# Kernel optimization log

Measured on AMD Instinct MI355X. Metric: run time of the kernel, lower is better.

The kernel has to match this reference:

```python
import jax, jax.numpy as jnp
import numpy as np

N_QUBITS = 8
N_LAYERS = 3
STATE_DIM = 2 ** N_QUBITS
BATCH = 16384


def _ry(angle):
    # angle: scalar or (B,) -> (2,2) or (B,2,2) complex64 RY matrix
    c = jnp.cos(angle / 2)
    s = jnp.sin(angle / 2)
    return jnp.stack([jnp.stack([c, -s], -1), jnp.stack([s, c], -1)], -2).astype(jnp.complex64)


def _rz(angle):
    # scalar angle -> (2,2) complex64 diag(e^{-i a/2}, e^{i a/2})
    return jnp.diag(jnp.stack([jnp.exp(-1j * angle / 2), jnp.exp(1j * angle / 2)])).astype(jnp.complex64)


def _apply_gate(state, qubit, gate):
    # state: (B, STATE_DIM) complex64; gate: (2,2) or (B,2,2) complex64
    # qubit 0 is the most-significant bit (matches torch view [B,2,...,2])
    B = state.shape[0]
    left = 2 ** qubit
    right = STATE_DIM // (2 * left)
    s = state.reshape(B, left, 2, right)
    if gate.ndim == 3:
        s = jnp.einsum('bst,batr->basr', gate, s)
    else:
        s = jnp.einsum('st,batr->basr', gate, s)
    return s.reshape(B, STATE_DIM)


def _cnot(state, control, target):
    # swap amplitudes with target bit flipped where control bit == 1;
    # identity when target == control (torch skips that case).
    idx = jnp.arange(STATE_DIM)
    cbit = (idx >> (N_QUBITS - 1 - control)) & 1
    tmask = jnp.left_shift(1, N_QUBITS - 1 - target)
    perm = jnp.where(cbit == 1, jnp.bitwise_xor(idx, tmask), idx)
    perm = jnp.where(target == control, idx, perm)
    return state[:, perm]


def _circuit(x, theta, omega, attn_w):
    B = x.shape[0]
    state = jnp.zeros((B, STATE_DIM), jnp.complex64).at[:, 0].set(1.0)
    # amplitude-angle encoding: per-sample RY on each qubit
    for i in range(N_QUBITS):
        state = _apply_gate(state, i, _ry(x[:, i]))
    # CNOT targets from softmax-argmax of entangle attention rows
    targets = jnp.argmax(jax.nn.softmax(attn_w, axis=1), axis=1)  # (N_QUBITS,)
    for layer in range(N_LAYERS):
        for i in range(N_QUBITS):
            state = _apply_gate(state, i, _ry(theta[layer, i]))
        for i in range(N_QUBITS):
            state = _cnot(state, i, targets[i])
        for i in range(N_QUBITS):
            state = _apply_gate(state, i, _rz(omega[layer, i]))
    return state


def setup_inputs() -> dict:
    key = jax.random.key(0)
    k1, k2, k3, k4 = jax.random.split(key, 4)
    x = jax.random.uniform(k1, (BATCH, N_QUBITS), jnp.float32) * np.float32(np.pi)
    theta = jax.random.normal(k2, (N_LAYERS, N_QUBITS), jnp.float32) * 0.1
    omega = jax.random.normal(k3, (N_LAYERS, N_QUBITS), jnp.float32) * 0.1
    # orthogonal init like nn.init.orthogonal_
    w = np.asarray(jax.random.normal(k4, (N_QUBITS, N_QUBITS), jnp.float32))
    q, r = np.linalg.qr(w)
    attn_w = jnp.asarray(q * np.sign(np.diag(r)), jnp.float32)
    return {'x': x, 'theta': theta, 'omega': omega, 'attn_w': attn_w}


def reference(x, theta, omega, attn_w):
    # returns (BATCH, STATE_DIM) complex64 quantum state amplitudes
    return _circuit(x, theta, omega, attn_w)
```

## Files before the change

### kernel.cpp

```cpp
#include <hip/hip_runtime.h>
#include <hip/hip_bf16.h>

#define NQ 8
#define DIM 256
#define NL 3
#define BATCH 16384

using bf16x8 = __attribute__((ext_vector_type(8))) short;
using f32x4  = __attribute__((ext_vector_type(4))) float;

static __device__ __forceinline__ unsigned short f2bf(float f) {
    union { __hip_bfloat16 b; unsigned short u; } cv;
    cv.b = __float2bfloat16(f);
    return cv.u;
}

#define RYPAIR(c0, c1)                                                  \
    {                                                                   \
        float lr = re[c0], li = im[c0], hr = re[c1], hi = im[c1];       \
        re[c0] = cc * lr - s * hr;  im[c0] = cc * li - s * hi;          \
        re[c1] = s * lr + cc * hr;  im[c1] = s * li + cc * hi;          \
    }

#define RUN_LAYERS()                                                              \
    for (int layer = 0; layer < NL; ++layer) {                                    \
        _Pragma("unroll")                                                         \
        for (int q = 0; q < NQ; ++q) {                                            \
            float a = 0.5f * theta[layer * NQ + q];                               \
            float s, cc; sincosf(a, &s, &cc);                                     \
            const int mask = 1 << (7 - q);                                        \
            if (mask == 128)      { RYPAIR(0, 2); RYPAIR(1, 3); }                 \
            else if (mask == 64)  { RYPAIR(0, 1); RYPAIR(2, 3); }                 \
            else {                                                                \
                _Pragma("unroll")                                                 \
                for (int c = 0; c < 4; ++c) {                                     \
                    float pr = __shfl_xor(re[c], mask);                           \
                    float pi = __shfl_xor(im[c], mask);                           \
                    if (lane & mask) { re[c] = s * pr + cc * re[c]; im[c] = s * pi + cc * im[c]; } \
                    else             { re[c] = cc * re[c] - s * pr; im[c] = cc * im[c] - s * pi; } \
                }                                                                 \
            }                                                                     \
        }                                                                         \
        _Pragma("unroll")                                                         \
        for (int i = 0; i < NQ; ++i) {                                            \
            int t2 = tgt[i];                                                      \
            if (t2 == i) continue;                                                \
            int cmask = 1 << (7 - i);                                             \
            int tmask = 1 << (7 - t2);                                            \
            if (tmask == 128) {                                                   \
                int j0 = lane, j1 = 64 + lane, j2 = 128 + lane, j3 = 192 + lane;  \
                bool k0 = (j0 & cmask), k1 = (j1 & cmask), k2 = (j2 & cmask), k3 = (j3 & cmask); \
                float n0r = k0 ? re[2] : re[0], n0i = k0 ? im[2] : im[0];         \
                float n1r = k1 ? re[3] : re[1], n1i = k1 ? im[3] : im[1];         \
                float n2r = k2 ? re[0] : re[2], n2i = k2 ? im[0] : im[2];         \
                float n3r = k3 ? re[1] : re[3], n3i = k3 ? im[1] : im[3];         \
                re[0] = n0r; im[0] = n0i; re[1] = n1r; im[1] = n1i;               \
                re[2] = n2r; im[2] = n2i; re[3] = n3r; im[3] = n3i;               \
            } else if (tmask == 64) {                                             \
                int j0 = lane, j1 = 64 + lane, j2 = 128 + lane, j3 = 192 + lane;  \
                bool k0 = (j0 & cmask), k1 = (j1 & cmask), k2 = (j2 & cmask), k3 = (j3 & cmask); \
                float n0r = k0 ? re[1] : re[0], n0i = k0 ? im[1] : im[0];         \
                float n1r = k1 ? re[0] : re[1], n1i = k1 ? im[0] : im[1];         \
                float n2r = k2 ? re[3] : re[2], n2i = k2 ? im[3] : im[2];         \
                float n3r = k3 ? re[2] : re[3], n3i = k3 ? im[2] : im[3];         \
                re[0] = n0r; im[0] = n0i; re[1] = n1r; im[1] = n1i;               \
                re[2] = n2r; im[2] = n2i; re[3] = n3r; im[3] = n3i;               \
            } else {                                                              \
                _Pragma("unroll")                                                 \
                for (int c = 0; c < 4; ++c) {                                     \
                    int j = c * 64 + lane;                                        \
                    float pr = __shfl_xor(re[c], tmask);                          \
                    float pi = __shfl_xor(im[c], tmask);                          \
                    bool take = (j & cmask) != 0;                                 \
                    re[c] = take ? pr : re[c];                                    \
                    im[c] = take ? pi : im[c];                                    \
                }                                                                 \
            }                                                                     \
        }                                                                         \
        _Pragma("unroll")                                                         \
        for (int q = 0; q < NQ; ++q) {                                            \
            float a = 0.5f * omega[layer * NQ + q];                               \
            float sa, ca; sincosf(a, &sa, &ca);                                   \
            const int mask = 1 << (7 - q);                                        \
            _Pragma("unroll")                                                     \
            for (int c = 0; c < 4; ++c) {                                         \
                int j = c * 64 + lane;                                            \
                float sb = (j & mask) ? sa : -sa;                                 \
                float r2 = re[c] * ca - im[c] * sb;                               \
                float i2 = re[c] * sb + im[c] * ca;                               \
                re[c] = r2; im[c] = i2;                                           \
            }                                                                     \
        }                                                                         \
    }

#define ARGMAX_TGT()                                                    \
    int tgt[NQ];                                                        \
    _Pragma("unroll")                                                   \
    for (int i = 0; i < NQ; ++i) {                                      \
        const float* row = attn_w + i * NQ;                             \
        int best = 0; float bv = row[0];                                \
        _Pragma("unroll")                                               \
        for (int t2 = 1; t2 < NQ; ++t2) {                               \
            float v = row[t2];                                          \
            if (v > bv) { bv = v; best = t2; }                          \
        }                                                               \
        tgt[i] = best;                                                  \
    }

__global__ __launch_bounds__(256) void build_B_kernel(
    const float* __restrict__ theta, const float* __restrict__ omega,
    const float* __restrict__ attn_w, unsigned short* __restrict__ Bf)
{
    const int lane = threadIdx.x & 63;
    const int k = blockIdx.x * 4 + (threadIdx.x >> 6);

    ARGMAX_TGT();

    float re[4], im[4];
    #pragma unroll
    for (int c = 0; c < 4; ++c) {
        re[c] = (c * 64 + lane == k) ? 1.0f : 0.0f;
        im[c] = 0.0f;
    }

    RUN_LAYERS();

    const int kbase = (k >> 5) * 32;
    const int lg16  = ((k >> 3) & 3) * 16;
    const int e     = k & 7;
    #pragma unroll
    for (int c = 0; c < 4; ++c) {
        int j  = c * 64 + lane;
        int n0 = 2 * j, n1 = 2 * j + 1;
        size_t o0 = ((size_t)(kbase + (n0 >> 4)) * 64 + lg16 + (n0 & 15)) * 8 + e;
        size_t o1 = ((size_t)(kbase + (n1 >> 4)) * 64 + lg16 + (n1 & 15)) * 8 + e;
        Bf[o0] = f2bf(im[c]);
        Bf[o1] = f2bf(re[c]);
    }
}

__global__ __launch_bounds__(512) void gemm_kernel(
    const float* __restrict__ x, const unsigned short* __restrict__ Bf,
    unsigned short* __restrict__ out)
{
    __shared__ unsigned short A_lds[64][264];
    __shared__ float trig[64][NQ][2];
    const int t = threadIdx.x;
    const int b0 = blockIdx.x * 64;

    {
        int b = t >> 3, q = t & 7;
        float a = 0.5f * x[(size_t)(b0 + b) * NQ + q];
        float s, c; sincosf(a, &s, &c);
        trig[b][q][0] = c; trig[b][q][1] = s;
    }
    __syncthreads();

    {
        int b = t >> 3;
        int j0 = (t & 7) * 32;
        float cq[NQ], sq[NQ];
        #pragma unroll
        for (int q = 0; q < NQ; ++q) { cq[q] = trig[b][q][0]; sq[q] = trig[b][q][1]; }
        float hi3 = (((j0 >> 7) & 1) ? sq[0] : cq[0]) *
                    (((j0 >> 6) & 1) ? sq[1] : cq[1]) *
                    (((j0 >> 5) & 1) ? sq[2] : cq[2]);
        float t3[8];
        #pragma unroll
        for (int h = 0; h < 8; ++h)
            t3[h] = ((h & 4) ? sq[3] : cq[3]) * ((h & 2) ? sq[4] : cq[4]) * ((h & 1) ? sq[5] : cq[5]);
        float t2v[4];
        #pragma unroll
        for (int v2 = 0; v2 < 4; ++v2)
            t2v[v2] = ((v2 & 2) ? sq[6] : cq[6]) * ((v2 & 1) ? sq[7] : cq[7]);
        #pragma unroll
        for (int i = 0; i < 32; i += 2) {
            float v0 = hi3 * t3[i >> 2] * t2v[i & 3];
            float v1 = hi3 * t3[(i + 1) >> 2] * t2v[(i + 1) & 3];
            unsigned int pack = (unsigned int)f2bf(v0) | ((unsigned int)f2bf(v1) << 16);
            *(unsigned int*)&A_lds[b][j0 + i] = pack;
        }
    }
    __syncthreads();

    const int w = t >> 6;
    const int l = t & 63;
    const int lrow = l & 15, lgrp = l >> 4;
    f32x4 acc[4][4];
    #pragma unroll
    for (int m = 0; m < 4; ++m)
        #pragma unroll
        for (int nt = 0; nt < 4; ++nt)
            acc[m][nt] = (f32x4){0.f, 0.f, 0.f, 0.f};

    #pragma unroll
    for (int ks = 0; ks < 8; ++ks) {
        bf16x8 bfrag[4];
        #pragma unroll
        for (int nt = 0; nt < 4; ++nt)
            bfrag[nt] = *(const bf16x8*)&Bf[((size_t)(ks * 32 + w * 4 + nt) * 64 + l) * 8];
        bf16x8 afrag[4];
        #pragma unroll
        for (int m = 0; m < 4; ++m)
            afrag[m] = *(const bf16x8*)&A_lds[m * 16 + lrow][ks * 32 + lgrp * 8];
        #pragma unroll
        for (int m = 0; m < 4; ++m)
            #pragma unroll
            for (int nt = 0; nt < 4; ++nt)
                acc[m][nt] = __builtin_amdgcn_mfma_f32_16x16x32_bf16(
                    afrag[m], bfrag[nt], acc[m][nt], 0, 0, 0);
    }

    #pragma unroll
    for (int m = 0; m < 4; ++m)
        #pragma unroll
        for (int nt = 0; nt < 4; ++nt)
            #pragma unroll
            for (int r = 0; r < 4; ++r) {
                int row = b0 + m * 16 + lgrp * 4 + r;
                int n = (w * 4 + nt) * 16 + lrow;
                out[(size_t)row * 512 + n] = f2bf(acc[m][nt][r]);
            }
}

__global__ __launch_bounds__(256) void sim_kernel(
    const float* __restrict__ x, const float* __restrict__ theta,
    const float* __restrict__ omega, const float* __restrict__ attn_w,
    unsigned short* __restrict__ out)
{
    const int lane = threadIdx.x & 63;
    const int b = blockIdx.x * 4 + (threadIdx.x >> 6);

    ARGMAX_TGT();

    float cq[NQ], sq[NQ];
    #pragma unroll
    for (int q = 0; q < NQ; ++q) {
        float a = 0.5f * x[(size_t)b * NQ + q];
        sincosf(a, &sq[q], &cq[q]);
    }
    float re[4], im[4];
    #pragma unroll
    for (int c = 0; c < 4; ++c) {
        int j = c * 64 + lane;
        float v = 1.0f;
        #pragma unroll
        for (int q = 0; q < NQ; ++q)
            v *= ((j >> (7 - q)) & 1) ? sq[q] : cq[q];
        re[c] = v; im[c] = 0.0f;
    }

    RUN_LAYERS();

    #pragma unroll
    for (int c = 0; c < 4; ++c) {
        size_t elem = (size_t)b * DIM + c * 64 + lane;
        unsigned int pack = (unsigned int)f2bf(im[c]) | ((unsigned int)f2bf(re[c]) << 16);
        *(unsigned int*)&out[elem * 2] = pack;
    }
}

extern "C" void kernel_launch(void* const* d_in, const int* in_sizes, int n_in,
                              void* d_out, int out_size, void* d_ws, size_t ws_size,
                              hipStream_t stream) {
    const float* x      = (const float*)d_in[0];
    const float* theta  = (const float*)d_in[1];
    const float* omega  = (const float*)d_in[2];
    const float* attn_w = (const float*)d_in[3];

    const size_t B_BYTES = (size_t)DIM * 512 * 2;
    if (ws_size >= B_BYTES) {
        unsigned short* Bf = (unsigned short*)d_ws;
        build_B_kernel<<<DIM / 4, 256, 0, stream>>>(theta, omega, attn_w, Bf);
        gemm_kernel<<<BATCH / 64, 512, 0, stream>>>(x, Bf, (unsigned short*)d_out);
    } else {
        sim_kernel<<<BATCH / 4, 256, 0, stream>>>(x, theta, omega, attn_w,
                                                  (unsigned short*)d_out);
    }
}
```

Baseline: 29.29 us.

## Fuse unitary build and GEMM into one cooperative kernel with grid sync

```diff
diff --git a/kernel.cpp b/kernel.cpp
--- a/kernel.cpp
+++ b/kernel.cpp
@@ -1,5 +1,8 @@
 #include <hip/hip_runtime.h>
 #include <hip/hip_bf16.h>
+#include <hip/hip_cooperative_groups.h>
+
+namespace cg = cooperative_groups;
 
 #define NQ 8
 #define DIM 256
@@ -22,12 +25,31 @@
         re[c1] = s * lr + cc * hr;  im[c1] = s * li + cc * hi;          \
     }
 
-#define RUN_LAYERS()                                                              \
+#define LOAD_TABLES()                                                   \
+    if (t < NL * NQ) {                                                  \
+        float s, c; sincosf(0.5f * theta[t], &s, &c);                   \
+        ths[t] = s; thc[t] = c;                                         \
+    } else if (t < 2 * NL * NQ) {                                       \
+        int i = t - NL * NQ;                                            \
+        float s, c; sincosf(0.5f * omega[i], &s, &c);                   \
+        oms[i] = s; omc[i] = c;                                         \
+    } else if (t < 2 * NL * NQ + NQ) {                                  \
+        int i = t - 2 * NL * NQ;                                        \
+        const float* row = attn_w + i * NQ;                             \
+        int best = 0; float bv = row[0];                                \
+        _Pragma("unroll")                                               \
+        for (int t2 = 1; t2 < NQ; ++t2) {                               \
+            float v = row[t2];                                          \
+            if (v > bv) { bv = v; best = t2; }                          \
+        }                                                               \
+        tgt_l[i] = best;                                                \
+    }
+
+#define RUN_LAYERS_LDS(LANE)                                                      \
     for (int layer = 0; layer < NL; ++layer) {                                    \
         _Pragma("unroll")                                                         \
         for (int q = 0; q < NQ; ++q) {                                            \
-            float a = 0.5f * theta[layer * NQ + q];                               \
-            float s, cc; sincosf(a, &s, &cc);                                     \
+            float s = ths[layer * NQ + q], cc = thc[layer * NQ + q];              \
             const int mask = 1 << (7 - q);                                        \
             if (mask == 128)      { RYPAIR(0, 2); RYPAIR(1, 3); }                 \
             else if (mask == 64)  { RYPAIR(0, 1); RYPAIR(2, 3); }                 \
@@ -36,19 +58,19 @@
                 for (int c = 0; c < 4; ++c) {                                     \
                     float pr = __shfl_xor(re[c], mask);                           \
                     float pi = __shfl_xor(im[c], mask);                           \
-                    if (lane & mask) { re[c] = s * pr + cc * re[c]; im[c] = s * pi + cc * im[c]; } \
-                    else             { re[c] = cc * re[c] - s * pr; im[c] = cc * im[c] - s * pi; } \
+                    if ((LANE) & mask) { re[c] = s * pr + cc * re[c]; im[c] = s * pi + cc * im[c]; } \
+                    else               { re[c] = cc * re[c] - s * pr; im[c] = cc * im[c] - s * pi; } \
                 }                                                                 \
             }                                                                     \
         }                                                                         \
         _Pragma("unroll")                                                         \
         for (int i = 0; i < NQ; ++i) {                                            \
-            int t2 = tgt[i];                                                      \
+            int t2 = tgt_l[i];                                                    \
             if (t2 == i) continue;                                                \
             int cmask = 1 << (7 - i);                                             \
             int tmask = 1 << (7 - t2);                                            \
             if (tmask == 128) {                                                   \
-                int j0 = lane, j1 = 64 + lane, j2 = 128 + lane, j3 = 192 + lane;  \
+                int j0 = (LANE), j1 = 64 + (LANE), j2 = 128 + (LANE), j3 = 192 + (LANE); \
                 bool k0 = (j0 & cmask), k1 = (j1 & cmask), k2 = (j2 & cmask), k3 = (j3 & cmask); \
                 float n0r = k0 ? re[2] : re[0], n0i = k0 ? im[2] : im[0];         \
                 float n1r = k1 ? re[3] : re[1], n1i = k1 ? im[3] : im[1];         \
@@ -57,7 +79,7 @@
                 re[0] = n0r; im[0] = n0i; re[1] = n1r; im[1] = n1i;               \
                 re[2] = n2r; im[2] = n2i; re[3] = n3r; im[3] = n3i;               \
             } else if (tmask == 64) {                                             \
-                int j0 = lane, j1 = 64 + lane, j2 = 128 + lane, j3 = 192 + lane;  \
+                int j0 = (LANE), j1 = 64 + (LANE), j2 = 128 + (LANE), j3 = 192 + (LANE); \
                 bool k0 = (j0 & cmask), k1 = (j1 & cmask), k2 = (j2 & cmask), k3 = (j3 & cmask); \
                 float n0r = k0 ? re[1] : re[0], n0i = k0 ? im[1] : im[0];         \
                 float n1r = k1 ? re[0] : re[1], n1i = k1 ? im[0] : im[1];         \
@@ -68,7 +90,7 @@
             } else {                                                              \
                 _Pragma("unroll")                                                 \
                 for (int c = 0; c < 4; ++c) {                                     \
-                    int j = c * 64 + lane;                                        \
+                    int j = c * 64 + (LANE);                                      \
                     float pr = __shfl_xor(re[c], tmask);                          \
                     float pi = __shfl_xor(im[c], tmask);                          \
                     bool take = (j & cmask) != 0;                                 \
@@ -79,12 +101,11 @@
         }                                                                         \
         _Pragma("unroll")                                                         \
         for (int q = 0; q < NQ; ++q) {                                            \
-            float a = 0.5f * omega[layer * NQ + q];                               \
-            float sa, ca; sincosf(a, &sa, &ca);                                   \
+            float sa = oms[layer * NQ + q], ca = omc[layer * NQ + q];             \
             const int mask = 1 << (7 - q);                                        \
             _Pragma("unroll")                                                     \
             for (int c = 0; c < 4; ++c) {                                         \
-                int j = c * 64 + lane;                                            \
+                int j = c * 64 + (LANE);                                          \
                 float sb = (j & mask) ? sa : -sa;                                 \
                 float r2 = re[c] * ca - im[c] * sb;                               \
                 float i2 = re[c] * sb + im[c] * ca;                               \
@@ -93,50 +114,152 @@
         }                                                                         \
     }
 
-#define ARGMAX_TGT()                                                    \
-    int tgt[NQ];                                                        \
-    _Pragma("unroll")                                                   \
-    for (int i = 0; i < NQ; ++i) {                                      \
-        const float* row = attn_w + i * NQ;                             \
-        int best = 0; float bv = row[0];                                \
+#define STORE_BF_SLICE(K, LANE)                                         \
+    {                                                                   \
+        const int kbase = ((K) >> 5) * 32;                              \
+        const int lg16  = (((K) >> 3) & 3) * 16;                        \
+        const int e     = (K) & 7;                                      \
         _Pragma("unroll")                                               \
-        for (int t2 = 1; t2 < NQ; ++t2) {                               \
-            float v = row[t2];                                          \
-            if (v > bv) { bv = v; best = t2; }                          \
+        for (int c = 0; c < 4; ++c) {                                   \
+            int j  = c * 64 + (LANE);                                   \
+            int n0 = 2 * j, n1 = 2 * j + 1;                             \
+            size_t o0 = ((size_t)(kbase + (n0 >> 4)) * 64 + lg16 + (n0 & 15)) * 8 + e; \
+            size_t o1 = ((size_t)(kbase + (n1 >> 4)) * 64 + lg16 + (n1 & 15)) * 8 + e; \
+            Bf[o0] = f2bf(im[c]);            \
+            Bf[o1] = f2bf(re[c]);                     \
         }                                                               \
-        tgt[i] = best;                                                  \
-    }
+    }
+
+#define STAGE_A()                                                                 \
+    {                                                                             \
+        int b = t >> 3, q = t & 7;                                                \
+        float a = 0.5f * x[(size_t)(b0 + b) * NQ + q];                            \
+        float s, c; sincosf(a, &s, &c);                                           \
+        trig[b][q][0] = c; trig[b][q][1] = s;                                     \
+    }                                                                             \
+    __syncthreads();                                                              \
+    {                                                                             \
+        int b = t >> 3;                                                           \
+        int j0 = (t & 7) * 32;                                                    \
+        float cq[NQ], sq[NQ];                                                     \
+        _Pragma("unroll")                                                         \
+        for (int q = 0; q < NQ; ++q) { cq[q] = trig[b][q][0]; sq[q] = trig[b][q][1]; } \
+        float hi3 = (((j0 >> 7) & 1) ? sq[0] : cq[0]) *                           \
+                    (((j0 >> 6) & 1) ? sq[1] : cq[1]) *                           \
+                    (((j0 >> 5) & 1) ? sq[2] : cq[2]);                            \
+        float t3[8];                                                              \
+        _Pragma("unroll")                                                         \
+        for (int h = 0; h < 8; ++h)                                               \
+            t3[h] = ((h & 4) ? sq[3] : cq[3]) * ((h & 2) ? sq[4] : cq[4]) * ((h & 1) ? sq[5] : cq[5]); \
+        float t2v[4];                                                             \
+        _Pragma("unroll")                                                         \
+        for (int v2 = 0; v2 < 4; ++v2)                                            \
+            t2v[v2] = ((v2 & 2) ? sq[6] : cq[6]) * ((v2 & 1) ? sq[7] : cq[7]);    \
+        _Pragma("unroll")                                                         \
+        for (int i = 0; i < 32; i += 2) {                                         \
+            float v0 = hi3 * t3[i >> 2] * t2v[i & 3];                             \
+            float v1 = hi3 * t3[(i + 1) >> 2] * t2v[(i + 1) & 3];                 \
+            unsigned int pack = (unsigned int)f2bf(v0) | ((unsigned int)f2bf(v1) << 16); \
+            *(unsigned int*)&A_lds[b][j0 + i] = pack;                             \
+        }                                                                         \
+    }
+
+#define MFMA_AND_STORE()                                                          \
+    {                                                                             \
+        const int w = t >> 6;                                                     \
+        const int l = t & 63;                                                     \
+        const int lrow = l & 15, lgrp = l >> 4;                                   \
+        f32x4 acc[4][4];                                                          \
+        _Pragma("unroll")                                                         \
+        for (int m = 0; m < 4; ++m)                                               \
+            _Pragma("unroll")                                                     \
+            for (int nt = 0; nt < 4; ++nt)                                        \
+                acc[m][nt] = (f32x4){0.f, 0.f, 0.f, 0.f};                         \
+        _Pragma("unroll")                                                         \
+        for (int ks = 0; ks < 8; ++ks) {                                          \
+            bf16x8 bfrag[4];                                                      \
+            _Pragma("unroll")                                                     \
+            for (int nt = 0; nt < 4; ++nt)                                        \
+                bfrag[nt] = *(const bf16x8*)&Bf[((size_t)(ks * 32 + w * 4 + nt) * 64 + l) * 8]; \
+            bf16x8 afrag[4];                                                      \
+            _Pragma("unroll")                                                     \
+            for (int m = 0; m < 4; ++m)                                           \
+                afrag[m] = *(const bf16x8*)&A_lds[m * 16 + lrow][ks * 32 + lgrp * 8]; \
+            _Pragma("unroll")                                                     \
+            for (int m = 0; m < 4; ++m)                                           \
+                _Pragma("unroll")                                                 \
+                for (int nt = 0; nt < 4; ++nt)                                    \
+                    acc[m][nt] = __builtin_amdgcn_mfma_f32_16x16x32_bf16(         \
+                        afrag[m], bfrag[nt], acc[m][nt], 0, 0, 0);                \
+        }                                                                         \
+        _Pragma("unroll")                                                         \
+        for (int m = 0; m < 4; ++m)                                               \
+            _Pragma("unroll")                                                     \
+            for (int nt = 0; nt < 4; ++nt)                                        \
+                _Pragma("unroll")                                                 \
+                for (int r = 0; r < 4; ++r) {                                     \
+                    int row = b0 + m * 16 + lgrp * 4 + r;                         \
+                    int n = (w * 4 + nt) * 16 + lrow;                             \
+                    out[(size_t)row * 512 + n] = f2bf(acc[m][nt][r]);             \
+                }                                                                 \
+    }
+
+__global__ __launch_bounds__(512) void fused_kernel(
+    const float* __restrict__ x, const float* __restrict__ theta,
+    const float* __restrict__ omega, const float* __restrict__ attn_w,
+    unsigned short* __restrict__ Bf, unsigned short* __restrict__ out)
+{
+    __shared__ unsigned short A_lds[64][264];
+    __shared__ float trig[64][NQ][2];
+    __shared__ float thc[NL * NQ], ths[NL * NQ], omc[NL * NQ], oms[NL * NQ];
+    __shared__ int   tgt_l[NQ];
+
+    const int t = threadIdx.x;
+    const int b0 = blockIdx.x * 64;
+
+    LOAD_TABLES();
+    STAGE_A();
+
+    if (t < 64) {
+        const int lane = t;
+        const int k = blockIdx.x;
+        float re[4], im[4];
+        #pragma unroll
+        for (int c = 0; c < 4; ++c) {
+            re[c] = (c * 64 + lane == k) ? 1.0f : 0.0f;
+            im[c] = 0.0f;
+        }
+        RUN_LAYERS_LDS(lane);
+        STORE_BF_SLICE(k, lane);
+    }
+
+    __threadfence();
+    cg::this_grid().sync();
+    __threadfence();
+
+    MFMA_AND_STORE();
+}
 
 __global__ __launch_bounds__(256) void build_B_kernel(
     const float* __restrict__ theta, const float* __restrict__ omega,
     const float* __restrict__ attn_w, unsigned short* __restrict__ Bf)
 {
-    const int lane = threadIdx.x & 63;
-    const int k = blockIdx.x * 4 + (threadIdx.x >> 6);
-
-    ARGMAX_TGT();
-
+    __shared__ float thc[NL * NQ], ths[NL * NQ], omc[NL * NQ], oms[NL * NQ];
+    __shared__ int   tgt_l[NQ];
+    const int t = threadIdx.x;
+    LOAD_TABLES();
+    __syncthreads();
+
+    const int lane = t & 63;
+    const int k = blockIdx.x * 4 + (t >> 6);
     float re[4], im[4];
     #pragma unroll
     for (int c = 0; c < 4; ++c) {
         re[c] = (c * 64 + lane == k) ? 1.0f : 0.0f;
         im[c] = 0.0f;
     }
-
-    RUN_LAYERS();
-
-    const int kbase = (k >> 5) * 32;
-    const int lg16  = ((k >> 3) & 3) * 16;
-    const int e     = k & 7;
-    #pragma unroll
-    for (int c = 0; c < 4; ++c) {
-        int j  = c * 64 + lane;
-        int n0 = 2 * j, n1 = 2 * j + 1;
-        size_t o0 = ((size_t)(kbase + (n0 >> 4)) * 64 + lg16 + (n0 & 15)) * 8 + e;
-        size_t o1 = ((size_t)(kbase + (n1 >> 4)) * 64 + lg16 + (n1 & 15)) * 8 + e;
-        Bf[o0] = f2bf(im[c]);
-        Bf[o1] = f2bf(re[c]);
-    }
+    RUN_LAYERS_LDS(lane);
+    STORE_BF_SLICE(k, lane);
 }
 
 __global__ __launch_bounds__(512) void gemm_kernel(
@@ -147,80 +270,9 @@
     __shared__ float trig[64][NQ][2];
     const int t = threadIdx.x;
     const int b0 = blockIdx.x * 64;
-
-    {
-        int b = t >> 3, q = t & 7;
-        float a = 0.5f * x[(size_t)(b0 + b) * NQ + q];
-        float s, c; sincosf(a, &s, &c);
-        trig[b][q][0] = c; trig[b][q][1] = s;
-    }
+    STAGE_A();
     __syncthreads();
-
-    {
-        int b = t >> 3;
-        int j0 = (t & 7) * 32;
-        float cq[NQ], sq[NQ];
-        #pragma unroll
-        for (int q = 0; q < NQ; ++q) { cq[q] = trig[b][q][0]; sq[q] = trig[b][q][1]; }
-        float hi3 = (((j0 >> 7) & 1) ? sq[0] : cq[0]) *
-                    (((j0 >> 6) & 1) ? sq[1] : cq[1]) *
-                    (((j0 >> 5) & 1) ? sq[2] : cq[2]);
-        float t3[8];
-        #pragma unroll
-        for (int h = 0; h < 8; ++h)
-            t3[h] = ((h & 4) ? sq[3] : cq[3]) * ((h & 2) ? sq[4] : cq[4]) * ((h & 1) ? sq[5] : cq[5]);
-        float t2v[4];
-        #pragma unroll
-        for (int v2 = 0; v2 < 4; ++v2)
-            t2v[v2] = ((v2 & 2) ? sq[6] : cq[6]) * ((v2 & 1) ? sq[7] : cq[7]);
-        #pragma unroll
-        for (int i = 0; i < 32; i += 2) {
-            float v0 = hi3 * t3[i >> 2] * t2v[i & 3];
-            float v1 = hi3 * t3[(i + 1) >> 2] * t2v[(i + 1) & 3];
-            unsigned int pack = (unsigned int)f2bf(v0) | ((unsigned int)f2bf(v1) << 16);
-            *(unsigned int*)&A_lds[b][j0 + i] = pack;
-        }
-    }
-    __syncthreads();
-
-    const int w = t >> 6;
-    const int l = t & 63;
-    const int lrow = l & 15, lgrp = l >> 4;
-    f32x4 acc[4][4];
-    #pragma unroll
-    for (int m = 0; m < 4; ++m)
-        #pragma unroll
-        for (int nt = 0; nt < 4; ++nt)
-            acc[m][nt] = (f32x4){0.f, 0.f, 0.f, 0.f};
-
-    #pragma unroll
-    for (int ks = 0; ks < 8; ++ks) {
-        bf16x8 bfrag[4];
-        #pragma unroll
-        for (int nt = 0; nt < 4; ++nt)
-            bfrag[nt] = *(const bf16x8*)&Bf[((size_t)(ks * 32 + w * 4 + nt) * 64 + l) * 8];
-        bf16x8 afrag[4];
-        #pragma unroll
-        for (int m = 0; m < 4; ++m)
-            afrag[m] = *(const bf16x8*)&A_lds[m * 16 + lrow][ks * 32 + lgrp * 8];
-        #pragma unroll
-        for (int m = 0; m < 4; ++m)
-            #pragma unroll
-            for (int nt = 0; nt < 4; ++nt)
-                acc[m][nt] = __builtin_amdgcn_mfma_f32_16x16x32_bf16(
-                    afrag[m], bfrag[nt], acc[m][nt], 0, 0, 0);
-    }
-
-    #pragma unroll
-    for (int m = 0; m < 4; ++m)
-        #pragma unroll
-        for (int nt = 0; nt < 4; ++nt)
-            #pragma unroll
-            for (int r = 0; r < 4; ++r) {
-                int row = b0 + m * 16 + lgrp * 4 + r;
-                int n = (w * 4 + nt) * 16 + lrow;
-                out[(size_t)row * 512 + n] = f2bf(acc[m][nt][r]);
-            }
+    MFMA_AND_STORE();
 }
 
 __global__ __launch_bounds__(256) void sim_kernel(
@@ -228,10 +280,14 @@
     const float* __restrict__ omega, const float* __restrict__ attn_w,
     unsigned short* __restrict__ out)
 {
-    const int lane = threadIdx.x & 63;
-    const int b = blockIdx.x * 4 + (threadIdx.x >> 6);
-
-    ARGMAX_TGT();
+    __shared__ float thc[NL * NQ], ths[NL * NQ], omc[NL * NQ], oms[NL * NQ];
+    __shared__ int   tgt_l[NQ];
+    const int t = threadIdx.x;
+    LOAD_TABLES();
+    __syncthreads();
+
+    const int lane = t & 63;
+    const int b = blockIdx.x * 4 + (t >> 6);
 
     float cq[NQ], sq[NQ];
     #pragma unroll
@@ -249,9 +305,7 @@
             v *= ((j >> (7 - q)) & 1) ? sq[q] : cq[q];
         re[c] = v; im[c] = 0.0f;
     }
-
-    RUN_LAYERS();
-
+    RUN_LAYERS_LDS(lane);
     #pragma unroll
     for (int c = 0; c < 4; ++c) {
         size_t elem = (size_t)b * DIM + c * 64 + lane;
@@ -267,14 +321,20 @@
     const float* theta  = (const float*)d_in[1];
     const float* omega  = (const float*)d_in[2];
     const float* attn_w = (const float*)d_in[3];
+    unsigned short* outp = (unsigned short*)d_out;
 
     const size_t B_BYTES = (size_t)DIM * 512 * 2;
     if (ws_size >= B_BYTES) {
         unsigned short* Bf = (unsigned short*)d_ws;
-        build_B_kernel<<<DIM / 4, 256, 0, stream>>>(theta, omega, attn_w, Bf);
-        gemm_kernel<<<BATCH / 64, 512, 0, stream>>>(x, Bf, (unsigned short*)d_out);
+        void* args[6] = { (void*)&x, (void*)&theta, (void*)&omega,
+                          (void*)&attn_w, (void*)&Bf, (void*)&outp };
+        hipError_t err = hipLaunchCooperativeKernel(
+            (const void*)fused_kernel, dim3(256), dim3(512), args, 0, stream);
+        if (err != hipSuccess) {
+            build_B_kernel<<<DIM / 4, 256, 0, stream>>>(theta, omega, attn_w, Bf);
+            gemm_kernel<<<BATCH / 64, 512, 0, stream>>>(x, Bf, outp);
+        }
     } else {
-        sim_kernel<<<BATCH / 4, 256, 0, stream>>>(x, theta, omega, attn_w,
-                                                  (unsigned short*)d_out);
-    }
-}
+        sim_kernel<<<BATCH / 4, 256, 0, stream>>>(x, theta, omega, attn_w, outp);
+    }
+}
```

After: 114.1 us. 289% more time.
